# Performance work log

Measured on AMD Instinct MI355X. Metric: run time of the kernel, lower is better.

Reference implementation:

```python
import jax, jax.numpy as jnp
import numpy as np

B, C, Ci = 4, 256, 128
T, H, W = 16, 28, 28
EPS = 1e-5  # BatchNorm eps


def conv1x1(x, w, b):
    # 1x1x1 Conv3d == channel-mixing GEMM. x: (b,c,t,h,w), w: (o,c), b: (o,)
    return jnp.einsum('bcthw,oc->bothw', x, w) + b[None, :, None, None, None]


def pool2(x):
    # MaxPool3d(kernel_size=2, stride=2); all spatial dims are even here.
    b, c, t, h, w = x.shape
    return x.reshape(b, c, t // 2, 2, h // 2, 2, w // 2, 2).max(axis=(3, 5, 7))


def setup_inputs() -> dict:
    key = jax.random.key(0)
    ks = jax.random.split(key, 9)
    kaiming_in = (2.0 / C) ** 0.5   # kaiming_normal_ fan_in for 1x1 conv
    kaiming_mid = (2.0 / Ci) ** 0.5
    return {
        'x': jax.random.normal(ks[0], (B, C, T, H, W), jnp.float32),
        'w_g': jax.random.normal(ks[1], (Ci, C), jnp.float32) * kaiming_in,
        'b_g': jnp.zeros((Ci,), jnp.float32),
        'w_theta': jax.random.normal(ks[2], (Ci, C), jnp.float32) * kaiming_in,
        'b_theta': jnp.zeros((Ci,), jnp.float32),
        'w_phi': jax.random.normal(ks[3], (Ci, C), jnp.float32) * kaiming_in,
        'b_phi': jnp.zeros((Ci,), jnp.float32),
        'w_W': jax.random.normal(ks[4], (C, Ci), jnp.float32) * kaiming_mid,
        'b_W': jnp.zeros((C,), jnp.float32),
        'bn_gamma': 1.0 + 0.1 * jax.random.normal(ks[5], (C,), jnp.float32),
        'bn_beta': 0.1 * jax.random.normal(ks[6], (C,), jnp.float32),
        'bn_mean': 0.1 * jax.random.normal(ks[7], (C,), jnp.float32),
        'bn_var': jax.random.uniform(ks[8], (C,), jnp.float32, 0.5, 1.5),
    }


def reference(x, w_g, b_g, w_theta, b_theta, w_phi, b_phi, w_W, b_W,
              bn_gamma, bn_beta, bn_mean, bn_var):
    b = x.shape[0]
    # g/phi are sub-sampled (MaxPool3d(2)) -> M = N/8 keys
    g_x = pool2(conv1x1(x, w_g, b_g)).reshape(b, Ci, -1).transpose(0, 2, 1)    # (b, M, Ci)
    theta_x = conv1x1(x, w_theta, b_theta).reshape(b, Ci, -1).transpose(0, 2, 1)  # (b, N, Ci)
    phi_x = pool2(conv1x1(x, w_phi, b_phi)).reshape(b, Ci, -1)                # (b, Ci, M)
    f = jnp.einsum('bnc,bcm->bnm', theta_x, phi_x)                            # (b, N, M)
    attn = jax.nn.softmax(f, axis=-1)
    y = jnp.einsum('bnm,bmc->bnc', attn, g_x)                                 # (b, N, Ci)
    y = y.transpose(0, 2, 1).reshape(b, Ci, T, H, W)
    W_y = conv1x1(y, w_W, b_W)
    # BatchNorm3d (eval mode with running stats)
    scale = (bn_gamma / jnp.sqrt(bn_var + EPS))[None, :, None, None, None]
    W_y = (W_y - bn_mean[None, :, None, None, None]) * scale + bn_beta[None, :, None, None, None]
    return W_y + x
```

## Files before the change

kernel.cpp:

```cpp
#include <hip/hip_runtime.h>
#include <math.h>

typedef _Float16 f16;
typedef _Float16 f16x8 __attribute__((ext_vector_type(8)));
typedef float f32x4 __attribute__((ext_vector_type(4)));
typedef float f32x16 __attribute__((ext_vector_type(16)));

#define BB 4
#define CC 256
#define CI 128
#define NN 12544
#define MM 1568
#define TP 8
#define HP 14
#define WP 14

#define OFF_W3T 0u
#define OFF_WWH 196608u
#define OFF_B3  262144u
#define OFF_SC  263168u
#define OFF_OFB 264192u
#define OFF_XT  265216u
#define OFF_TPG (OFF_XT + 25690112u)
#define OFF_PHI (OFF_TPG + 38535168u)
#define OFF_G   (OFF_PHI + 1605632u)
#define OFF_Y   (OFF_G + 1605632u)
#define WS_NEED (OFF_Y + 12845056u)
#define OFF_Y1  OFF_XT
#define OFF_ML  (OFF_XT + 12845056u)

static __device__ __forceinline__ f32x4 mfma16(f16x8 a, f16x8 b, f32x4 c) {
    return __builtin_amdgcn_mfma_f32_16x16x32_f16(a, b, c, 0, 0, 0);
}
static __device__ __forceinline__ f32x16 mfma32(f16x8 a, f16x8 b, f32x16 c) {
    return __builtin_amdgcn_mfma_f32_32x32x16_f16(a, b, c, 0, 0, 0);
}
static __device__ __forceinline__ unsigned pkrtz(float a, float b) {
    auto h = __builtin_amdgcn_cvt_pkrtz(a, b);
    return __builtin_bit_cast(unsigned, h);
}
static __device__ __forceinline__ void gload16(const f16* g, f16* l) {
    __builtin_amdgcn_global_load_lds((const __attribute__((address_space(1))) void*)g,
                                     (__attribute__((address_space(3))) void*)l, 16, 0, 0);
}

__global__ __launch_bounds__(256) void k_prep(
    const float* __restrict__ wg, const float* __restrict__ bg,
    const float* __restrict__ wth, const float* __restrict__ bth_,
    const float* __restrict__ wph, const float* __restrict__ bph,
    const float* __restrict__ wW, const float* __restrict__ bW,
    const float* __restrict__ gam, const float* __restrict__ bet,
    const float* __restrict__ mean, const float* __restrict__ var,
    f16* __restrict__ w3t, f16* __restrict__ wWh, f16* __restrict__ b3,
    float* __restrict__ sc, float* __restrict__ ofb) {
    int r = blockIdx.x;
    int c = threadIdx.x;
    const float* src = (r < 128) ? (wth + (size_t)r * CC)
                     : (r < 256) ? (wph + (size_t)(r - 128) * CC)
                                 : (wg + (size_t)(r - 256) * CC);
    w3t[(size_t)r * CC + c] = (f16)src[c];
    if (c == 0) {
        float bv = (r < 128) ? bth_[r] : (r < 256) ? bph[r - 128] : bg[r - 256];
        b3[r] = (f16)bv;
    }
    if (r < 256) {
        if (c < 128) wWh[(size_t)r * CI + c] = (f16)wW[(size_t)r * CI + c];
        if (c == 0) {
            float s = gam[r] * rsqrtf(var[r] + 1e-5f);
            sc[r] = s;
            ofb[r] = (bW[r] - mean[r]) * s + bet[r];
        }
    }
}

__global__ __launch_bounds__(256) void k_xt(const float* __restrict__ x, f16* __restrict__ xT) {
    int bid = blockIdx.x;
    int b = bid / (196 * 4); int rem = bid % (196 * 4);
    int nt = rem / 4, ct = rem % 4;
    int n0 = nt * 64, c0 = ct * 64;
    __shared__ float tile[64][65];
    const float* xb = x + (size_t)b * CC * NN;
    for (int p = 0; p < 16; ++p) {
        int idx = p * 256 + threadIdx.x;
        int i = idx >> 6, j = idx & 63;
        tile[i][j] = xb[(size_t)(c0 + i) * NN + n0 + j];
    }
    __syncthreads();
    f16* xTb = xT + (size_t)b * NN * CC;
    for (int p = 0; p < 16; ++p) {
        int idx = p * 256 + threadIdx.x;
        int n = idx >> 6, c = idx & 63;
        xTb[(size_t)(n0 + n) * CC + c0 + c] = (f16)tile[c][n];
    }
}

__global__ __launch_bounds__(256) void k_conv(const f16* __restrict__ xT, const f16* __restrict__ w3t,
                                              const f16* __restrict__ b3, f16* __restrict__ tpg) {
    int bid = blockIdx.x;
    int b = bid / (98 * 3); int rem = bid % (98 * 3);
    int nt = rem / 3, ct = rem % 3;
    int n0 = nt * 128, co0 = ct * 128;
    __shared__ f16 As[128 * 64];
    __shared__ f16 Bs[128 * 64];
    const f16* xb = xT + (size_t)b * NN * CC + (size_t)n0 * CC;
    const f16* wb = w3t + (size_t)co0 * CC;
    int wv = threadIdx.x >> 6, ln = threadIdx.x & 63;
    int wr = (wv & 1) * 64, wc = (wv >> 1) * 64;
    f32x4 acc[4][4];
    for (int i = 0; i < 4; ++i) for (int j = 0; j < 4; ++j)
        for (int r = 0; r < 4; ++r) acc[i][j][r] = 0.f;
    for (int ks = 0; ks < 4; ++ks) {
        for (int s = threadIdx.x; s < 1024; s += 256) {
            int row = s >> 3, sl = s & 7;
            f16x8 va = *(const f16x8*)(xb + (size_t)row * CC + ks * 64 + sl * 8);
            *(f16x8*)(As + row * 64 + ((sl * 8) ^ ((row & 7) << 3))) = va;
            f16x8 vb = *(const f16x8*)(wb + (size_t)row * CC + ks * 64 + sl * 8);
            *(f16x8*)(Bs + row * 64 + ((sl * 8) ^ ((row & 7) << 3))) = vb;
        }
        __syncthreads();
        for (int kc = 0; kc < 2; ++kc) {
            int klo = kc * 32 + ((ln >> 4) * 8);
            f16x8 af[4], bf[4];
            for (int i = 0; i < 4; ++i) {
                int rn = wr + i * 16 + (ln & 15);
                af[i] = *(const f16x8*)(As + rn * 64 + (klo ^ ((rn & 7) << 3)));
                int rc = wc + i * 16 + (ln & 15);
                bf[i] = *(const f16x8*)(Bs + rc * 64 + (klo ^ ((rc & 7) << 3)));
            }
            for (int i = 0; i < 4; ++i)
                for (int j = 0; j < 4; ++j)
                    acc[i][j] = mfma16(af[i], bf[j], acc[i][j]);
        }
        __syncthreads();
    }
    f16* ob = tpg + (size_t)b * NN * 384 + (size_t)n0 * 384 + co0;
    for (int j = 0; j < 4; ++j) {
        float bias = (float)b3[co0 + wc + j * 16 + (ln & 15)];
        for (int i = 0; i < 4; ++i)
            for (int r = 0; r < 4; ++r) {
                int n = wr + i * 16 + (ln >> 4) * 4 + r;
                int co = wc + j * 16 + (ln & 15);
                ob[(size_t)n * 384 + co] = (f16)(acc[i][j][r] + bias);
            }
    }
}

__global__ __launch_bounds__(256) void k_pool(const f16* __restrict__ tpg,
                                              f16* __restrict__ phi, f16* __restrict__ gx) {
    int bid = blockIdx.x;
    int b = bid / (TP * HP); int rem = bid % (TP * HP);
    int tp = rem / HP, hp = rem % HP;
    const f16* base = tpg + (size_t)b * NN * 384;
    for (int idx = threadIdx.x; idx < WP * 128; idx += 256) {
        int wp = idx >> 7, ci = idx & 127;
        f16 mp = (f16)(-60000.0f), mg = (f16)(-60000.0f);
        for (int dt = 0; dt < 2; ++dt)
            for (int dh = 0; dh < 2; ++dh)
                for (int dw = 0; dw < 2; ++dw) {
                    int n = (2 * tp + dt) * 784 + (2 * hp + dh) * 28 + (2 * wp + dw);
                    f16 vp = base[(size_t)n * 384 + 128 + ci];
                    f16 vg = base[(size_t)n * 384 + 256 + ci];
                    mp = vp > mp ? vp : mp;
                    mg = vg > mg ? vg : mg;
                }
        int m = tp * 196 + hp * 14 + wp;
        phi[(size_t)b * MM * CI + (size_t)m * CI + ci] = mp;
        gx[(size_t)b * CI * MM + (size_t)ci * MM + m] = mg;
    }
}


static __device__ __forceinline__ void dma_chunk(f16* __restrict__ buf,
        const f16* __restrict__ psrc, const f16* __restrict__ gsrc, int wv) {
    #pragma unroll
    for (int u = 0; u < 2; ++u) {
        int i = wv * 2 + u;
        gload16(psrc + i * 16, buf + i * 512);
        gload16(gsrc + (size_t)(i & 1) * 64 * MM + (i >> 1) * 8, buf + 4096 + i * 512);
    }
}

static __device__ __forceinline__ void sm_pv(f32x16& qk, const f16* __restrict__ Bg,
        f32x16* __restrict__ yv, float& mrun, float& lrun, int lq, int hi) {
    float t[8];
    #pragma unroll
    for (int i = 0; i < 8; ++i) t[i] = fmaxf(qk[i], qk[i + 8]);
    #pragma unroll
    for (int s = 4; s >= 1; s >>= 1)
        #pragma unroll
        for (int i = 0; i < s; ++i) t[i] = fmaxf(t[i], t[i + s]);
    float mx = fmaxf(t[0], __shfl_xor(t[0], 32));
    if (__any(mx > mrun + 8.f)) {
        float mnew = fmaxf(mrun, mx);
        float scl = __expf(mrun - mnew);
        lrun *= scl;
        #pragma unroll
        for (int c = 0; c < 4; ++c)
            #pragma unroll
            for (int r = 0; r < 16; ++r) yv[c][r] *= scl;
        mrun = mnew;
    }
    float ps = 0.f;
    #pragma unroll
    for (int r = 0; r < 16; ++r) {
        float p = __expf(qk[r] - mrun);
        qk[r] = p;
        ps += p;
    }
    ps += __shfl_xor(ps, 32);
    lrun += ps;
    #pragma unroll
    for (int s = 0; s < 2; ++s) {
        const int base = s * 8;
        unsigned A0 = pkrtz(qk[base + 0], qk[base + 1]);
        unsigned A1 = pkrtz(qk[base + 2], qk[base + 3]);
        unsigned B0 = pkrtz(qk[base + 4], qk[base + 5]);
        unsigned B1 = pkrtz(qk[base + 6], qk[base + 7]);
        unsigned g0 = (unsigned)__shfl_xor((int)(hi ? A0 : B0), 32);
        unsigned g1 = (unsigned)__shfl_xor((int)(hi ? A1 : B1), 32);
        union { unsigned u[4]; f16x8 v; } fr;
        fr.u[0] = hi ? g0 : A0;
        fr.u[1] = hi ? g1 : A1;
        fr.u[2] = hi ? B0 : g0;
        fr.u[3] = hi ? B1 : g1;
        __builtin_amdgcn_s_setprio(1);
        #pragma unroll
        for (int c = 0; c < 4; ++c) {
            f16x8 gfr = *(const f16x8*)(Bg + (s * 2 + hi) * 1024 + (c * 32 + lq) * 8);
            yv[c] = mfma32(gfr, fr.v, yv[c]);
        }
        __builtin_amdgcn_s_setprio(0);
    }
}

__global__ __launch_bounds__(256, 2) void k_attn(const f16* __restrict__ tpg, const f16* __restrict__ phi,
                                                 const f16* __restrict__ gx, f16* __restrict__ y0,
                                                 f16* __restrict__ y1, float2* __restrict__ ml) {
    int bid = blockIdx.x;
    int b = bid / 196; int rem = bid % 196;
    int nt = rem >> 1, kk = rem & 1;
    int n0 = nt * 128;
    __shared__ f16 BUF[2][8192];
    int tid = threadIdx.x;
    int wv = tid >> 6, l = tid & 63, hi = l >> 5, lq = l & 31;
    int n = n0 + wv * 32 + lq;
    f16x8 bth[8];
    {
        const f16* rowp = tpg + ((size_t)b * NN + n) * 384;
        #pragma unroll
        for (int ks = 0; ks < 8; ++ks)
            bth[ks] = *(const f16x8*)(rowp + ks * 16 + hi * 8);
    }
    f32x16 yv[4];
    #pragma unroll
    for (int c = 0; c < 4; ++c)
        #pragma unroll
        for (int r = 0; r < 16; ++r) yv[c][r] = 0.f;
    float mrun = -1e30f, lrun = 0.f;
    const f16* phib = phi + (size_t)b * MM * CI;
    const f16* gb = gx + (size_t)b * CI * MM;
    const f16* pbase = phib + (size_t)lq * CI + hi * 8;
    const f16* gbase = gb + (size_t)l * MM;
    int mstart = kk ? 768 : 0;
    int NC = 24 + kk;

    dma_chunk(BUF[0], pbase + (size_t)mstart * CI, gbase + mstart, wv);
    __syncthreads();
    for (int t = 0; t < NC; ++t) {
        if (t + 1 < NC) {
            int m1 = mstart + (t + 1) * 32;
            dma_chunk(BUF[(t + 1) & 1], pbase + (size_t)m1 * CI, gbase + m1, wv);
        }
        const f16* Bp = BUF[t & 1];
        f32x16 qk;
        #pragma unroll
        for (int r = 0; r < 16; ++r) qk[r] = 0.f;
        __builtin_amdgcn_s_setprio(1);
        #pragma unroll
        for (int ks = 0; ks < 8; ++ks) {
            f16x8 A = *(const f16x8*)(Bp + (2 * ks + hi) * 256 + lq * 8);
            qk = mfma32(A, bth[ks], qk);
        }
        __builtin_amdgcn_s_setprio(0);
        sm_pv(qk, Bp + 4096, yv, mrun, lrun, lq, hi);
        __syncthreads();
    }

    float inv = 1.f / lrun;
    f16* yb = (kk ? y1 : y0) + ((size_t)b * NN + n) * CI;
    #pragma unroll
    for (int c = 0; c < 4; ++c)
        #pragma unroll
        for (int k = 0; k < 4; ++k) {
            int ci = c * 32 + k * 8 + hi * 4;
            uint2 st;
            st.x = pkrtz(yv[c][4 * k + 0] * inv, yv[c][4 * k + 1] * inv);
            st.y = pkrtz(yv[c][4 * k + 2] * inv, yv[c][4 * k + 3] * inv);
            *(uint2*)(yb + ci) = st;
        }
    if (hi == 0) {
        float2 v; v.x = mrun; v.y = lrun;
        ml[((size_t)b * 2 + kk) * NN + n] = v;
    }
}

__global__ __launch_bounds__(256) void k_out(const f16* __restrict__ wWh, const f16* __restrict__ y0,
                                             const f16* __restrict__ y1, const float2* __restrict__ ml,
                                             const float* __restrict__ x, const float* __restrict__ sc,
                                             const float* __restrict__ ofb, float* __restrict__ out) {
    int bid = blockIdx.x;
    int b = bid / (196 * 2); int rem = bid % (196 * 2);
    int nt = rem >> 1, ct = rem & 1;
    int n0 = nt * 64, co0 = ct * 128;
    __shared__ f16 Ws[128 * 128];
    __shared__ f16 Ys[64 * 128];
    for (int s = threadIdx.x; s < 128 * 16; s += 256) {
        int row = s >> 4, sl = s & 15;
        f16x8 v = *(const f16x8*)(wWh + (size_t)(co0 + row) * CI + sl * 8);
        *(f16x8*)(Ws + row * 128 + ((sl * 8) ^ ((row & 7) << 3))) = v;
    }
    const size_t ybase = (size_t)b * NN * CI + (size_t)n0 * CI;
    const float2* mlb = ml + (size_t)b * 2 * NN;
    for (int s = threadIdx.x; s < 64 * 16; s += 256) {
        int row = s >> 4, sl = s & 15;
        int n = n0 + row;
        float2 m0 = mlb[n];
        float2 m1 = mlb[NN + n];
        float M = fmaxf(m0.x, m1.x);
        float e0 = __expf(m0.x - M) * m0.y;
        float e1 = __expf(m1.x - M) * m1.y;
        float iL = 1.f / (e0 + e1);
        float w0 = e0 * iL, w1 = e1 * iL;
        f16x8 v0 = *(const f16x8*)(y0 + ybase + (size_t)row * CI + sl * 8);
        f16x8 v1 = *(const f16x8*)(y1 + ybase + (size_t)row * CI + sl * 8);
        union { unsigned u[4]; f16x8 v; } o;
        #pragma unroll
        for (int j = 0; j < 4; ++j)
            o.u[j] = pkrtz(w0 * (float)v0[2 * j] + w1 * (float)v1[2 * j],
                           w0 * (float)v0[2 * j + 1] + w1 * (float)v1[2 * j + 1]);
        *(f16x8*)(Ys + row * 128 + ((sl * 8) ^ ((row & 7) << 3))) = o.v;
    }
    __syncthreads();
    int wv = threadIdx.x >> 6, ln = threadIdx.x & 63;
    int wc = (wv >> 1) * 64, wn = (wv & 1) * 32;
    f32x4 acc[4][2];
    for (int i = 0; i < 4; ++i) for (int j = 0; j < 2; ++j)
        for (int r = 0; r < 4; ++r) acc[i][j][r] = 0.f;
    for (int kc = 0; kc < 4; ++kc) {
        int klo = kc * 32 + (ln >> 4) * 8;
        f16x8 afr[4], bfr[2];
        for (int i = 0; i < 4; ++i) {
            int rc = wc + i * 16 + (ln & 15);
            afr[i] = *(const f16x8*)(Ws + rc * 128 + (klo ^ ((rc & 7) << 3)));
        }
        for (int j = 0; j < 2; ++j) {
            int rn = wn + j * 16 + (ln & 15);
            bfr[j] = *(const f16x8*)(Ys + rn * 128 + (klo ^ ((rn & 7) << 3)));
        }
        for (int i = 0; i < 4; ++i)
            for (int j = 0; j < 2; ++j)
                acc[i][j] = mfma16(afr[i], bfr[j], acc[i][j]);
    }
    const float* xb = x + (size_t)b * CC * NN;
    float* ob = out + (size_t)b * CC * NN;
    for (int i = 0; i < 4; ++i)
        for (int j = 0; j < 2; ++j)
            for (int r = 0; r < 4; ++r) {
                int co = co0 + wc + i * 16 + (ln >> 4) * 4 + r;
                int n = n0 + wn + j * 16 + (ln & 15);
                size_t idx = (size_t)co * NN + n;
                ob[idx] = acc[i][j][r] * sc[co] + ofb[co] + xb[idx];
            }
}

extern "C" void kernel_launch(void* const* d_in, const int* in_sizes, int n_in,
                              void* d_out, int out_size, void* d_ws, size_t ws_size,
                              hipStream_t stream) {
    const float* x    = (const float*)d_in[0];
    const float* wg   = (const float*)d_in[1];
    const float* bg   = (const float*)d_in[2];
    const float* wth  = (const float*)d_in[3];
    const float* bth  = (const float*)d_in[4];
    const float* wph  = (const float*)d_in[5];
    const float* bph  = (const float*)d_in[6];
    const float* wW   = (const float*)d_in[7];
    const float* bW   = (const float*)d_in[8];
    const float* gam  = (const float*)d_in[9];
    const float* bet  = (const float*)d_in[10];
    const float* mean = (const float*)d_in[11];
    const float* var  = (const float*)d_in[12];
    if (ws_size < (size_t)WS_NEED) return;
    char* ws = (char*)d_ws;
    f16* w3t = (f16*)(ws + OFF_W3T);
    f16* wWh = (f16*)(ws + OFF_WWH);
    f16* b3  = (f16*)(ws + OFF_B3);
    float* sc  = (float*)(ws + OFF_SC);
    float* ofb = (float*)(ws + OFF_OFB);
    f16* xT  = (f16*)(ws + OFF_XT);
    f16* tpg = (f16*)(ws + OFF_TPG);
    f16* phi = (f16*)(ws + OFF_PHI);
    f16* gx  = (f16*)(ws + OFF_G);
    f16* yy0 = (f16*)(ws + OFF_Y);
    f16* yy1 = (f16*)(ws + OFF_Y1);
    float2* ml = (float2*)(ws + OFF_ML);
    float* out = (float*)d_out;

    k_prep<<<dim3(384), dim3(256), 0, stream>>>(wg, bg, wth, bth, wph, bph, wW, bW,
                                                gam, bet, mean, var, w3t, wWh, b3, sc, ofb);
    k_xt  <<<dim3(BB * 196 * 4), dim3(256), 0, stream>>>(x, xT);
    k_conv<<<dim3(BB * 98 * 3), dim3(256), 0, stream>>>(xT, w3t, b3, tpg);
    k_pool<<<dim3(BB * TP * HP), dim3(256), 0, stream>>>(tpg, phi, gx);
    k_attn<<<dim3(BB * 98 * 2), dim3(256), 0, stream>>>(tpg, phi, gx, yy0, yy1, ml);
    k_out <<<dim3(BB * 196 * 2), dim3(256), 0, stream>>>(wWh, yy0, yy1, ml, x, sc, ofb, out);
}
```

Baseline: 160.0 us.

## Split attention key range into four partitions and separate theta from phi/g storage

The attention kernel now splits the 1568 keys into four partitions (13/12/12/12 chunks) instead of two, doubling the grid so the GPU is filled more evenly. The output kernel merges four partial results using their per-row max and sum statistics. The conv output is also split into a dense theta buffer and a phi/g buffer, so theta rows are read with a 128 stride instead of a 384 stride. The trade-off is extra partial-output traffic and four-way merge work in the output kernel, and more reused workspace regions.

Measured after the change: 163.5 us. 1.02x slower.

```diff
diff --git a/kernel.cpp b/kernel.cpp
--- a/kernel.cpp
+++ b/kernel.cpp
@@ -21,12 +21,15 @@
 #define OFF_SC  263168u
 #define OFF_OFB 264192u
 #define OFF_XT  265216u
-#define OFF_TPG (OFF_XT + 25690112u)
-#define OFF_PHI (OFF_TPG + 38535168u)
+#define OFF_TH  (OFF_XT + 25690112u)
+#define OFF_PG  (OFF_TH + 12845056u)
+#define OFF_PHI (OFF_PG + 25690112u)
 #define OFF_G   (OFF_PHI + 1605632u)
 #define OFF_Y   (OFF_G + 1605632u)
 #define WS_NEED (OFF_Y + 12845056u)
-#define OFF_Y1  OFF_XT
+#define OFF_Y1  OFF_PG
+#define OFF_Y2  (OFF_PG + 12845056u)
+#define OFF_Y3  OFF_XT
 #define OFF_ML  (OFF_XT + 12845056u)
 
 static __device__ __forceinline__ f32x4 mfma16(f16x8 a, f16x8 b, f32x4 c) {
@@ -95,7 +98,8 @@
 }
 
 __global__ __launch_bounds__(256) void k_conv(const f16* __restrict__ xT, const f16* __restrict__ w3t,
-                                              const f16* __restrict__ b3, f16* __restrict__ tpg) {
+                                              const f16* __restrict__ b3, f16* __restrict__ th,
+                                              f16* __restrict__ pg) {
     int bid = blockIdx.x;
     int b = bid / (98 * 3); int rem = bid % (98 * 3);
     int nt = rem / 3, ct = rem % 3;
@@ -133,24 +137,26 @@
         }
         __syncthreads();
     }
-    f16* ob = tpg + (size_t)b * NN * 384 + (size_t)n0 * 384 + co0;
+    f16* ob; int ostr;
+    if (ct == 0) { ob = th + (size_t)b * NN * 128 + (size_t)n0 * 128; ostr = 128; }
+    else         { ob = pg + (size_t)b * NN * 256 + (size_t)n0 * 256 + (ct - 1) * 128; ostr = 256; }
     for (int j = 0; j < 4; ++j) {
         float bias = (float)b3[co0 + wc + j * 16 + (ln & 15)];
         for (int i = 0; i < 4; ++i)
             for (int r = 0; r < 4; ++r) {
                 int n = wr + i * 16 + (ln >> 4) * 4 + r;
                 int co = wc + j * 16 + (ln & 15);
-                ob[(size_t)n * 384 + co] = (f16)(acc[i][j][r] + bias);
+                ob[(size_t)n * ostr + co] = (f16)(acc[i][j][r] + bias);
             }
     }
 }
 
-__global__ __launch_bounds__(256) void k_pool(const f16* __restrict__ tpg,
+__global__ __launch_bounds__(256) void k_pool(const f16* __restrict__ pg,
                                               f16* __restrict__ phi, f16* __restrict__ gx) {
     int bid = blockIdx.x;
     int b = bid / (TP * HP); int rem = bid % (TP * HP);
     int tp = rem / HP, hp = rem % HP;
-    const f16* base = tpg + (size_t)b * NN * 384;
+    const f16* base = pg + (size_t)b * NN * 256;
     for (int idx = threadIdx.x; idx < WP * 128; idx += 256) {
         int wp = idx >> 7, ci = idx & 127;
         f16 mp = (f16)(-60000.0f), mg = (f16)(-60000.0f);
@@ -158,8 +164,8 @@
             for (int dh = 0; dh < 2; ++dh)
                 for (int dw = 0; dw < 2; ++dw) {
                     int n = (2 * tp + dt) * 784 + (2 * hp + dh) * 28 + (2 * wp + dw);
-                    f16 vp = base[(size_t)n * 384 + 128 + ci];
-                    f16 vg = base[(size_t)n * 384 + 256 + ci];
+                    f16 vp = base[(size_t)n * 256 + ci];
+                    f16 vg = base[(size_t)n * 256 + 128 + ci];
                     mp = vp > mp ? vp : mp;
                     mg = vg > mg ? vg : mg;
                 }
@@ -233,12 +239,13 @@
     }
 }
 
-__global__ __launch_bounds__(256, 2) void k_attn(const f16* __restrict__ tpg, const f16* __restrict__ phi,
+__global__ __launch_bounds__(256, 2) void k_attn(const f16* __restrict__ th, const f16* __restrict__ phi,
                                                  const f16* __restrict__ gx, f16* __restrict__ y0,
-                                                 f16* __restrict__ y1, float2* __restrict__ ml) {
+                                                 f16* __restrict__ y1, f16* __restrict__ y2,
+                                                 f16* __restrict__ y3, float2* __restrict__ ml) {
     int bid = blockIdx.x;
-    int b = bid / 196; int rem = bid % 196;
-    int nt = rem >> 1, kk = rem & 1;
+    int b = bid / 392; int rem = bid % 392;
+    int nt = rem >> 2, kk = rem & 3;
     int n0 = nt * 128;
     __shared__ f16 BUF[2][8192];
     int tid = threadIdx.x;
@@ -246,7 +253,7 @@
     int n = n0 + wv * 32 + lq;
     f16x8 bth[8];
     {
-        const f16* rowp = tpg + ((size_t)b * NN + n) * 384;
+        const f16* rowp = th + ((size_t)b * NN + n) * 128;
         #pragma unroll
         for (int ks = 0; ks < 8; ++ks)
             bth[ks] = *(const f16x8*)(rowp + ks * 16 + hi * 8);
@@ -261,8 +268,8 @@
     const f16* gb = gx + (size_t)b * CI * MM;
     const f16* pbase = phib + (size_t)lq * CI + hi * 8;
     const f16* gbase = gb + (size_t)l * MM;
-    int mstart = kk ? 768 : 0;
-    int NC = 24 + kk;
+    int mstart = (kk == 0) ? 0 : (416 + (kk - 1) * 384);
+    int NC = (kk == 0) ? 13 : 12;
 
     dma_chunk(BUF[0], pbase + (size_t)mstart * CI, gbase + mstart, wv);
     __syncthreads();
@@ -287,7 +294,8 @@
     }
 
     float inv = 1.f / lrun;
-    f16* yb = (kk ? y1 : y0) + ((size_t)b * NN + n) * CI;
+    f16* ypart = (kk == 0) ? y0 : (kk == 1) ? y1 : (kk == 2) ? y2 : y3;
+    f16* yb = ypart + ((size_t)b * NN + n) * CI;
     #pragma unroll
     for (int c = 0; c < 4; ++c)
         #pragma unroll
@@ -300,12 +308,13 @@
         }
     if (hi == 0) {
         float2 v; v.x = mrun; v.y = lrun;
-        ml[((size_t)b * 2 + kk) * NN + n] = v;
+        ml[((size_t)b * 4 + kk) * NN + n] = v;
     }
 }
 
 __global__ __launch_bounds__(256) void k_out(const f16* __restrict__ wWh, const f16* __restrict__ y0,
-                                             const f16* __restrict__ y1, const float2* __restrict__ ml,
+                                             const f16* __restrict__ y1, const f16* __restrict__ y2,
+                                             const f16* __restrict__ y3, const float2* __restrict__ ml,
                                              const float* __restrict__ x, const float* __restrict__ sc,
                                              const float* __restrict__ ofb, float* __restrict__ out) {
     int bid = blockIdx.x;
@@ -320,24 +329,29 @@
         *(f16x8*)(Ws + row * 128 + ((sl * 8) ^ ((row & 7) << 3))) = v;
     }
     const size_t ybase = (size_t)b * NN * CI + (size_t)n0 * CI;
-    const float2* mlb = ml + (size_t)b * 2 * NN;
+    const float2* mlb = ml + (size_t)b * 4 * NN;
     for (int s = threadIdx.x; s < 64 * 16; s += 256) {
         int row = s >> 4, sl = s & 15;
         int n = n0 + row;
-        float2 m0 = mlb[n];
-        float2 m1 = mlb[NN + n];
-        float M = fmaxf(m0.x, m1.x);
-        float e0 = __expf(m0.x - M) * m0.y;
-        float e1 = __expf(m1.x - M) * m1.y;
-        float iL = 1.f / (e0 + e1);
-        float w0 = e0 * iL, w1 = e1 * iL;
-        f16x8 v0 = *(const f16x8*)(y0 + ybase + (size_t)row * CI + sl * 8);
-        f16x8 v1 = *(const f16x8*)(y1 + ybase + (size_t)row * CI + sl * 8);
+        float2 q0 = mlb[n], q1 = mlb[NN + n], q2 = mlb[2 * NN + n], q3 = mlb[3 * NN + n];
+        float M = fmaxf(fmaxf(q0.x, q1.x), fmaxf(q2.x, q3.x));
+        float e0 = __expf(q0.x - M) * q0.y;
+        float e1 = __expf(q1.x - M) * q1.y;
+        float e2 = __expf(q2.x - M) * q2.y;
+        float e3 = __expf(q3.x - M) * q3.y;
+        float iL = 1.f / (e0 + e1 + e2 + e3);
+        float w0 = e0 * iL, w1 = e1 * iL, w2 = e2 * iL, w3 = e3 * iL;
+        size_t off = ybase + (size_t)row * CI + sl * 8;
+        f16x8 v0 = *(const f16x8*)(y0 + off);
+        f16x8 v1 = *(const f16x8*)(y1 + off);
+        f16x8 v2 = *(const f16x8*)(y2 + off);
+        f16x8 v3 = *(const f16x8*)(y3 + off);
         union { unsigned u[4]; f16x8 v; } o;
         #pragma unroll
         for (int j = 0; j < 4; ++j)
-            o.u[j] = pkrtz(w0 * (float)v0[2 * j] + w1 * (float)v1[2 * j],
-                           w0 * (float)v0[2 * j + 1] + w1 * (float)v1[2 * j + 1]);
+            o.u[j] = pkrtz(
+                w0 * (float)v0[2 * j] + w1 * (float)v1[2 * j] + w2 * (float)v2[2 * j] + w3 * (float)v3[2 * j],
+                w0 * (float)v0[2 * j + 1] + w1 * (float)v1[2 * j + 1] + w2 * (float)v2[2 * j + 1] + w3 * (float)v3[2 * j + 1]);
         *(f16x8*)(Ys + row * 128 + ((sl * 8) ^ ((row & 7) << 3))) = o.v;
     }
     __syncthreads();
@@ -397,19 +411,22 @@
     float* sc  = (float*)(ws + OFF_SC);
     float* ofb = (float*)(ws + OFF_OFB);
     f16* xT  = (f16*)(ws + OFF_XT);
-    f16* tpg = (f16*)(ws + OFF_TPG);
+    f16* th  = (f16*)(ws + OFF_TH);
+    f16* pg  = (f16*)(ws + OFF_PG);
     f16* phi = (f16*)(ws + OFF_PHI);
     f16* gx  = (f16*)(ws + OFF_G);
     f16* yy0 = (f16*)(ws + OFF_Y);
     f16* yy1 = (f16*)(ws + OFF_Y1);
+    f16* yy2 = (f16*)(ws + OFF_Y2);
+    f16* yy3 = (f16*)(ws + OFF_Y3);
     float2* ml = (float2*)(ws + OFF_ML);
     float* out = (float*)d_out;
 
     k_prep<<<dim3(384), dim3(256), 0, stream>>>(wg, bg, wth, bth, wph, bph, wW, bW,
                                                 gam, bet, mean, var, w3t, wWh, b3, sc, ofb);
     k_xt  <<<dim3(BB * 196 * 4), dim3(256), 0, stream>>>(x, xT);
-    k_conv<<<dim3(BB * 98 * 3), dim3(256), 0, stream>>>(xT, w3t, b3, tpg);
-    k_pool<<<dim3(BB * TP * HP), dim3(256), 0, stream>>>(tpg, phi, gx);
-    k_attn<<<dim3(BB * 98 * 2), dim3(256), 0, stream>>>(tpg, phi, gx, yy0, yy1, ml);
-    k_out <<<dim3(BB * 196 * 2), dim3(256), 0, stream>>>(wWh, yy0, yy1, ml, x, sc, ofb, out);
-}
+    k_conv<<<dim3(BB * 98 * 3), dim3(256), 0, stream>>>(xT, w3t, b3, th, pg);
+    k_pool<<<dim3(BB * TP * HP), dim3(256), 0, stream>>>(pg, phi, gx);
+    k_attn<<<dim3(BB * 98 * 4), dim3(256), 0, stream>>>(th, phi, gx, yy0, yy1, yy2, yy3, ml);
+    k_out <<<dim3(BB * 196 * 2), dim3(256), 0, stream>>>(wWh, yy0, yy1, yy2, yy3, ml, x, sc, ofb, out);
+}
```
